# Optimization experiments

Measured on AMD Instinct MI355X. Metric: run time of the kernel, lower is better.

The kernel has to match this reference:

```python
import jax, jax.numpy as jnp
from jax import lax
import numpy as np

B, CIN, COUT, T, H, W, KH, KW = 8, 256, 256, 16, 28, 28, 3, 3


def setup_inputs() -> dict:
    key = jax.random.key(0)
    k1, k2, k3 = jax.random.split(key, 3)
    x = jax.random.normal(k1, (B, CIN, T, H, W), dtype=jnp.float32)
    alpha = jax.random.uniform(k2, (B, CIN, T, 1, 1), dtype=jnp.float32)
    # base weight, kaiming-uniform-like init, stored as [1,1,c_out,c_in,kh,kw]
    fan_in = CIN * KH * KW
    bound = 1.0 / np.sqrt(fan_in)
    weight = jax.random.uniform(k3, (1, 1, COUT, CIN, KH, KW), dtype=jnp.float32,
                                minval=-bound, maxval=bound)
    return {"x": x, "alpha": alpha, "weight": weight}


def reference(x, alpha, weight):
    # x: [b, c_in, t, h, w]; alpha: [b, c_in, t, 1, 1]; weight: [1,1,c_out,c_in,kh,kw]
    b, c_in, t, h, w = x.shape
    c_out = weight.shape[2]
    w_base = weight[0, 0]  # [c_out, c_in, kh, kw]
    # W_t = alpha_t * W_base scales only input channels (alpha broadcasts over c_out),
    # so (alpha*W) conv x == W conv (alpha*x): modulate input, then one shared conv.
    xm = x * alpha  # [b, c_in, t, h, w]
    xm = jnp.transpose(xm, (0, 2, 1, 3, 4)).reshape(b * t, c_in, h, w)
    y = lax.conv_general_dilated(
        xm, w_base,
        window_strides=(1, 1),
        padding=((1, 1), (1, 1)),
        dimension_numbers=("NCHW", "OIHW", "NCHW"),
    )  # [b*t, c_out, h, w]
    oh, ow = y.shape[-2], y.shape[-1]
    y = y.reshape(b, t, c_out, oh, ow)
    return jnp.transpose(y, (0, 2, 1, 3, 4))  # [b, c_out, t, h, w]
```

## Files before the change

kernel.cpp:

```cpp
#include <hip/hip_runtime.h>
#include <hip/hip_bf16.h>
#include <cstdint>

#define CIN   256
#define COUT  256
#define NB    8
#define NT    16
#define NH    28
#define NW    28
#define HP    30
#define WP    30

#define XM_ELEMS   ((size_t)NB * NT * HP * WP * CIN)
#define XM_BYTES   (XM_ELEMS * 2)

typedef __bf16 bf16x8 __attribute__((ext_vector_type(8)));
typedef float  f32x4  __attribute__((ext_vector_type(4)));

#define AS1 __attribute__((address_space(1)))
#define AS3 __attribute__((address_space(3)))

static __device__ __forceinline__ unsigned short f2bf(float f) {
    __hip_bfloat16 h = __float2bfloat16(f);
    return __builtin_bit_cast(unsigned short, h);
}

__global__ void modulate_kernel(const float* __restrict__ x,
                                const float* __restrict__ alpha,
                                unsigned short* __restrict__ xm) {
    const int ci = threadIdx.x;
    const int blk = blockIdx.x;
    const int hp = blk % 30;
    const int bt = blk / 30;
    unsigned short* row = xm + (size_t)(bt * 900 + hp * 30) * 256;
    if (hp == 0 || hp == 29) {
        #pragma unroll
        for (int wp = 0; wp < 30; ++wp) row[wp * 256 + ci] = 0;
        return;
    }
    const int t = bt & 15, b = bt >> 4;
    const int h = hp - 1;
    const float a = alpha[(b * CIN + ci) * NT + t];
    const float* xrow = x + ((size_t)((b * CIN + ci) * NT + t) * NH + h) * NW;
    row[ci] = 0;
    row[29 * 256 + ci] = 0;
    const float4* xv = (const float4*)xrow;
    #pragma unroll
    for (int q = 0; q < 7; ++q) {
        float4 v = xv[q];
        row[(q * 4 + 1) * 256 + ci] = f2bf(v.x * a);
        row[(q * 4 + 2) * 256 + ci] = f2bf(v.y * a);
        row[(q * 4 + 3) * 256 + ci] = f2bf(v.z * a);
        row[(q * 4 + 4) * 256 + ci] = f2bf(v.w * a);
    }
}

__global__ void repack_w_kernel(const float* __restrict__ w,
                                unsigned short* __restrict__ wB) {
    const int ci = threadIdx.x;
    const int tap = blockIdx.x >> 8;
    const int co  = blockIdx.x & 255;
    wB[((tap * 256 + co) * 256) + ci] = f2bf(w[(co * 256 + ci) * 9 + tap]);
}


#define BAR()    __builtin_amdgcn_s_barrier()
#define LGKM0()  asm volatile("s_waitcnt lgkmcnt(0)" ::: "memory")
#define VMW(N)   asm volatile("s_waitcnt vmcnt(" #N ")" ::: "memory")
#define SCHED0() __builtin_amdgcn_sched_barrier(0)
#define PRIO(x)  __builtin_amdgcn_s_setprio(x)

#define STAGE_F(P) do {                                                       \
    const int kh2 = (tap2 * 11) >> 5;                                         \
    const int kw2 = tap2 - 3 * kh2;                                           \
    const int aOff = tap2 * 65536 + cic2 * 32;                                \
    const int bOff = ((kh2 - 1) * 30 + (kw2 - 1)) * 256 + cic2 * 32;          \
    _Pragma("unroll") for (int c_ = 0; c_ < 2; ++c_)                          \
        __builtin_amdgcn_global_load_lds(                                     \
            (const AS1 void*)(aSrc + aOff + c_ * 32768),                      \
            (AS3 void*)(lds + (P)*32768 + (c_*128 + wave*16)*64 + lane*16),   \
            16, 0, 0);                                                        \
    _Pragma("unroll") for (int c_ = 0; c_ < 2; ++c_)                          \
        __builtin_amdgcn_global_load_lds(                                     \
            (const AS1 void*)(bL[c_] + bOff),                                 \
            (AS3 void*)(lds + (P)*32768 + 16384 + (c_*128 + wave*16)*64 + lane*16), \
            16, 0, 0);                                                        \
    if (++tap2 == 9) { tap2 = 0; ++cic2; }                                    \
} while (0)

#define READF(S, P) do {                                                      \
    _Pragma("unroll") for (int m_ = 0; m_ < 4; ++m_)                          \
        fa##S[m_] = *(const bf16x8*)(lds + (P)*32768 +                        \
            (wm*64 + m_*16 + l15)*64 + readSwz);                              \
    _Pragma("unroll") for (int f_ = 0; f_ < 7; ++f_)                          \
        fb##S[f_] = *(const bf16x8*)(lds + (P)*32768 + 16384 +                \
            (wn*112 + f_*16 + l15)*64 + readSwz);                             \
} while (0)

#define MFMA28(S) do {                                                        \
    _Pragma("unroll") for (int m_ = 0; m_ < 4; ++m_)                          \
    _Pragma("unroll") for (int f_ = 0; f_ < 7; ++f_)                          \
        acc[m_][f_] = __builtin_amdgcn_mfma_f32_16x16x32_bf16(                \
            fb##S[f_], fa##S[m_], acc[m_][f_], 0, 0, 0);                      \
} while (0)

__global__ __launch_bounds__(512, 2) void conv_gemm_kernel(
    const unsigned short* __restrict__ xm,
    const unsigned short* __restrict__ wB,
    float* __restrict__ out) {
    __shared__ __align__(1024) char lds[65536];

    const int tid  = threadIdx.x;
    const int wave = tid >> 6;
    const int lane = tid & 63;
    const int l15  = lane & 15;
    const int n0   = blockIdx.x * 224;
    const int wm   = wave >> 1;
    const int wn   = wave & 1;

    const int swzE = 8 * ((lane & 3) ^ ((lane >> 3) & 3));
    const unsigned short* aSrc = wB + (wave * 16 + (lane >> 2)) * 256 + swzE;

    const unsigned short* bL[2];
    #pragma unroll
    for (int c_ = 0; c_ < 2; ++c_) {
        int nl = c_ * 128 + wave * 16 + (lane >> 2);
        nl = nl > 223 ? 223 : nl;
        const int n  = n0 + nl;
        const int w_ = n % 28, h_ = (n / 28) % 28, bt = n / 784;
        bL[c_] = xm + (size_t)((bt * 30 + h_ + 1) * 30 + (w_ + 1)) * 256 + swzE;
    }

    const int readSwz = ((lane >> 4) ^ ((l15 >> 1) & 3)) << 4;

    f32x4 acc[4][7];
    #pragma unroll
    for (int i = 0; i < 4; ++i)
        #pragma unroll
        for (int j = 0; j < 7; ++j) acc[i][j] = f32x4{0.f, 0.f, 0.f, 0.f};

    bf16x8 faA[4], fbA[7], faB[4], fbB[7];

    int tap2 = 0, cic2 = 0;
    STAGE_F(0);
    STAGE_F(1);
    VMW(4);
    SCHED0();
    BAR();
    READF(A, 0);
    LGKM0();

    #pragma unroll 1
    for (int it = 0; it < 35; ++it) {
        VMW(0);
        SCHED0();
        BAR();
        READF(B, 1);
        STAGE_F(0);
        SCHED0();
        PRIO(1); MFMA28(A); PRIO(0);
        LGKM0();
        SCHED0();
        VMW(0);
        SCHED0();
        BAR();
        READF(A, 0);
        STAGE_F(1);
        SCHED0();
        PRIO(1); MFMA28(B); PRIO(0);
        LGKM0();
        SCHED0();
    }
    VMW(0);
    SCHED0();
    BAR();
    READF(B, 1);
    SCHED0();
    PRIO(1); MFMA28(A); PRIO(0);
    LGKM0();
    SCHED0();
    PRIO(1); MFMA28(B); PRIO(0);

    #pragma unroll
    for (int f = 0; f < 7; ++f) {
        const int n  = n0 + wn * 112 + f * 16 + ((lane >> 4) << 2);
        const int bt = n / 784;
        const int hw = n - bt * 784;
        const int b = bt >> 4, t = bt & 15;
        float* obase = out + ((size_t)(b * 256) * 16 + t) * 784 + hw;
        #pragma unroll
        for (int m = 0; m < 4; ++m) {
            const int co = wm * 64 + m * 16 + l15;
            *(f32x4*)(obase + (size_t)co * 12544) = acc[m][f];
        }
    }
}

extern "C" void kernel_launch(void* const* d_in, const int* in_sizes, int n_in,
                              void* d_out, int out_size, void* d_ws, size_t ws_size,
                              hipStream_t stream) {
    const float* x      = (const float*)d_in[0];
    const float* alpha  = (const float*)d_in[1];
    const float* weight = (const float*)d_in[2];
    float* out = (float*)d_out;

    unsigned short* xm = (unsigned short*)d_ws;
    unsigned short* wB = (unsigned short*)((char*)d_ws + XM_BYTES);

    modulate_kernel<<<dim3(NB * NT * HP), dim3(256), 0, stream>>>(x, alpha, xm);
    repack_w_kernel<<<dim3(9 * 256), dim3(256), 0, stream>>>(weight, wB);
    conv_gemm_kernel<<<dim3(448), dim3(512), 0, stream>>>(xm, wB, out);
}
```

Baseline: 167.0 us.

## Triple-buffer LDS stages in conv GEMM to prefetch two stages ahead

Grows the shared-memory staging from two to three buffers. Each step now waits with vmcnt(4) instead of draining all global-to-LDS loads, so one stage's loads can still be in flight while the next stage is read and its MFMAs run. The main loop is unrolled by six so the buffer rotation stays static, with a custom prologue and epilogue covering the 72 K-stages. The cost is 96 KB of LDS per block, which likely no longer allows the two resident blocks per CU that launch_bounds(512,2) asks for, so the 448-block grid may need a second wave of blocks.

```diff
diff --git a/kernel.cpp b/kernel.cpp
--- a/kernel.cpp
+++ b/kernel.cpp
@@ -104,11 +104,34 @@
             fb##S[f_], fa##S[m_], acc[m_][f_], 0, 0, 0);                      \
 } while (0)
 
+#define BODY_S(CS, NS, NBUF, SBUF) do {                                       \
+    VMW(4);                                                                   \
+    SCHED0();                                                                 \
+    BAR();                                                                    \
+    READF(NS, NBUF);                                                          \
+    STAGE_F(SBUF);                                                            \
+    SCHED0();                                                                 \
+    PRIO(1); MFMA28(CS); PRIO(0);                                             \
+    LGKM0();                                                                  \
+    SCHED0();                                                                 \
+} while (0)
+
+#define BODY_N(CS, NS, NBUF, VMN) do {                                        \
+    VMW(VMN);                                                                 \
+    SCHED0();                                                                 \
+    BAR();                                                                    \
+    READF(NS, NBUF);                                                          \
+    SCHED0();                                                                 \
+    PRIO(1); MFMA28(CS); PRIO(0);                                             \
+    LGKM0();                                                                  \
+    SCHED0();                                                                 \
+} while (0)
+
 __global__ __launch_bounds__(512, 2) void conv_gemm_kernel(
     const unsigned short* __restrict__ xm,
     const unsigned short* __restrict__ wB,
     float* __restrict__ out) {
-    __shared__ __align__(1024) char lds[65536];
+    __shared__ __align__(1024) char lds[98304];
 
     const int tid  = threadIdx.x;
     const int wave = tid >> 6;
@@ -144,41 +167,28 @@
     int tap2 = 0, cic2 = 0;
     STAGE_F(0);
     STAGE_F(1);
-    VMW(4);
+    STAGE_F(2);
+    VMW(8);
     SCHED0();
     BAR();
     READF(A, 0);
     LGKM0();
+    SCHED0();
 
     #pragma unroll 1
-    for (int it = 0; it < 35; ++it) {
-        VMW(0);
-        SCHED0();
-        BAR();
-        READF(B, 1);
-        STAGE_F(0);
-        SCHED0();
-        PRIO(1); MFMA28(A); PRIO(0);
-        LGKM0();
-        SCHED0();
-        VMW(0);
-        SCHED0();
-        BAR();
-        READF(A, 0);
-        STAGE_F(1);
-        SCHED0();
-        PRIO(1); MFMA28(B); PRIO(0);
-        LGKM0();
-        SCHED0();
-    }
-    VMW(0);
-    SCHED0();
-    BAR();
-    READF(B, 1);
-    SCHED0();
-    PRIO(1); MFMA28(A); PRIO(0);
-    LGKM0();
-    SCHED0();
+    for (int it = 0; it < 11; ++it) {
+        BODY_S(A, B, 1, 0);
+        BODY_S(B, A, 2, 1);
+        BODY_S(A, B, 0, 2);
+        BODY_S(B, A, 1, 0);
+        BODY_S(A, B, 2, 1);
+        BODY_S(B, A, 0, 2);
+    }
+    BODY_S(A, B, 1, 0);
+    BODY_S(B, A, 2, 1);
+    BODY_S(A, B, 0, 2);
+    BODY_N(B, A, 1, 4);
+    BODY_N(A, B, 2, 0);
     PRIO(1); MFMA28(B); PRIO(0);
 
     #pragma unroll
```

Result: faster. 158.3 us (-5.2%).
